# Optimization experiments

Hardware: AMD Instinct MI355X
Metric: run time of the kernel (lower is better)

## Reference

```python
import jax, jax.numpy as jnp
import numpy as np

N = 100000   # nodes
E = 3200000  # edges (avg degree 32)
BN_EPS = 1e-5


def setup_inputs() -> dict:
    key = jax.random.key(0)
    ks = jax.random.split(key, 24)
    w = lambda k, shape: jax.random.normal(k, shape, jnp.float32) * 0.05
    inp = {
        "x": jax.random.normal(ks[0], (N, 1), jnp.float32),
        "edge_index": jax.random.randint(ks[1], (2, E), 0, N, dtype=jnp.int32),
        # GINConv1 mlp1: Linear(1,256) -> BN(256) -> ReLU -> Linear(256,128)
        "w1a": w(ks[2], (1, 256)), "b1a": w(ks[3], (256,)),
        "g1": jnp.ones((256,), jnp.float32), "be1": w(ks[4], (256,)),
        "m1": w(ks[5], (256,)), "v1": jax.random.uniform(ks[6], (256,), jnp.float32, 0.5, 1.5),
        "w1b": w(ks[7], (256, 128)), "b1b": w(ks[8], (128,)),
        # GINConv2 mlp2: Linear(128,64) -> BN(64) -> ReLU -> Linear(64,64)
        "w2a": w(ks[9], (128, 64)), "b2a": w(ks[10], (64,)),
        "g2": jnp.ones((64,), jnp.float32), "be2": w(ks[11], (64,)),
        "m2": w(ks[12], (64,)), "v2": jax.random.uniform(ks[13], (64,), jnp.float32, 0.5, 1.5),
        "w2b": w(ks[14], (64, 64)), "b2b": w(ks[15], (64,)),
        # head: Linear(64,16) -> ReLU -> Linear(16,6) -> log_softmax
        "wl1": w(ks[16], (64, 16)), "bl1": w(ks[17], (16,)),
        "wl2": w(ks[18], (16, 6)), "bl2": w(ks[19], (6,)),
    }
    return inp


def _bn_eval(h, g, b, m, v):
    # BatchNorm1d in eval mode: running stats
    return (h - m) * jax.lax.rsqrt(v + BN_EPS) * g + b


def reference(x, edge_index, w1a, b1a, g1, be1, m1, v1, w1b, b1b,
              w2a, b2a, g2, be2, m2, v2, w2b, b2b, wl1, bl1, wl2, bl2):
    src, dst = edge_index[0], edge_index[1]
    n = x.shape[0]

    def gin(h, mlp):
        # GINConv (eps=0): mlp(h + sum_{j in N(i)} h_j)
        agg = jax.ops.segment_sum(h[src], dst, num_segments=n)
        return mlp(h + agg)

    mlp1 = lambda h: jnp.maximum(_bn_eval(h @ w1a + b1a, g1, be1, m1, v1), 0.0) @ w1b + b1b
    mlp2 = lambda h: jnp.maximum(_bn_eval(h @ w2a + b2a, g2, be2, m2, v2), 0.0) @ w2b + b2b

    x = gin(x, mlp1)   # [N,128]; dropout is identity in eval mode
    x = gin(x, mlp2)   # [N,64]
    x = jnp.maximum(x @ wl1 + bl1, 0.0)  # [N,16]
    x = x @ wl2 + bl2                    # [N,6]
    return jax.nn.log_softmax(x, axis=1)
```

## Files before the change

### kernel.cpp

```cpp
#include <hip/hip_runtime.h>
#include <stdint.h>

#define BN_EPS 1e-5f
#define BW    256
#define BSH   8
#define SLACK 10240
#define TILE  4096

static __device__ __forceinline__ uint32_t bf16bits(float f){
  uint32_t u = __float_as_uint(f);
  return (u + 0x7fffu + ((u>>16)&1u)) >> 16;
}
static __device__ __forceinline__ float bf16tof(uint32_t us){
  return __uint_as_float(us<<16);
}
static __device__ __forceinline__ void acc8(float* acc, uint4 v){
  acc[0]+=bf16tof(v.x&0xFFFFu); acc[1]+=bf16tof(v.x>>16);
  acc[2]+=bf16tof(v.y&0xFFFFu); acc[3]+=bf16tof(v.y>>16);
  acc[4]+=bf16tof(v.z&0xFFFFu); acc[5]+=bf16tof(v.z>>16);
  acc[6]+=bf16tof(v.w&0xFFFFu); acc[7]+=bf16tof(v.w>>16);
}

__global__ __launch_bounds__(256) void prep_small(const float* __restrict__ w1a, const float* __restrict__ b1a,
                           const float* __restrict__ g1,  const float* __restrict__ be1,
                           const float* __restrict__ m1,  const float* __restrict__ v1,
                           const float* __restrict__ b1b, const float* __restrict__ w2a,
                           const float* __restrict__ b2a, const float* __restrict__ g2,
                           const float* __restrict__ be2, const float* __restrict__ m2,
                           const float* __restrict__ v2,
                           float* __restrict__ a1, float* __restrict__ b1v,
                           float* __restrict__ c12, float* __restrict__ A2, float* __restrict__ B2,
                           float* __restrict__ sorted_p, int* __restrict__ perm){
  __shared__ float bpl[256];
  int c = threadIdx.x;
  float s1 = g1[c] * rsqrtf(v1[c] + BN_EPS);
  float av = w1a[c] * s1;
  float bv = (b1a[c] - m1[c]) * s1 + be1[c];
  a1[c]  = av;
  b1v[c] = bv;
  if (c < 64){
    float acc = 0.f;
    for (int d = 0; d < 128; ++d) acc = fmaf(b1b[d], w2a[d*64 + c], acc);
    c12[c] = acc;
    float s2 = g2[c] * rsqrtf(v2[c] + BN_EPS);
    A2[c] = s2;
    B2[c] = (b2a[c] - m2[c]) * s2 + be2[c];
  }
  float bp;
  if (av == 0.f) bp = 1e30f;
  else bp = fminf(fmaxf(-bv/av, -1e30f), 1e30f);
  bpl[c] = bp;
  __syncthreads();
  int rank = 0;
  for (int j = 0; j < 256; ++j){
    float bj = bpl[j];
    rank += (bj < bp) || (bj == bp && j < c);
  }
  sorted_p[rank] = bp;
  perm[rank] = c;
}

__global__ void prep_w12(const float* __restrict__ w1b, const float* __restrict__ w2a,
                         float* __restrict__ W12){
  int idx = blockIdx.x*256 + threadIdx.x;
  int c = idx >> 6, k = idx & 63;
  float acc = 0.f;
  for (int d = 0; d < 128; ++d) acc = fmaf(w1b[c*128 + d], w2a[d*64 + k], acc);
  W12[idx] = acc;
}

__global__ __launch_bounds__(256) void build_ab_par(const float* __restrict__ a1, const float* __restrict__ b1v,
                                                    const float* __restrict__ W12, const float* __restrict__ c12,
                                                    const int* __restrict__ perm, float* __restrict__ AB){
  __shared__ float sm[256];
  int col = blockIdx.x;
  int k = col & 63;
  bool isA = col < 64;
  int tm = threadIdx.x;
  float a0 = a1[tm], b0 = b1v[tm];
  float w0 = W12[tm*64 + k];
  bool act0 = (a0 < 0.f) || (a0 == 0.f && b0 > 0.f);
  float coeff0 = isA ? a0 : b0;
  sm[tm] = act0 ? coeff0*w0 : 0.f;
  __syncthreads();
  for (int off2 = 128; off2 > 0; off2 >>= 1){
    if (tm < off2) sm[tm] += sm[tm + off2];
    __syncthreads();
  }
  float base = sm[0] + (isA ? 0.f : c12[k]);
  __syncthreads();
  int g = perm[tm];
  float ag = a1[g], bg = b1v[g];
  float wg = W12[g*64 + k];
  float cg = isA ? ag : bg;
  float delta = (ag > 0.f) ? cg*wg : ((ag < 0.f) ? -cg*wg : 0.f);
  sm[tm] = delta;
  __syncthreads();
  for (int off = 1; off < 256; off <<= 1){
    float v = (tm >= off) ? sm[tm-off] : 0.f;
    __syncthreads();
    sm[tm] += v;
    __syncthreads();
  }
  AB[(tm+1)*128 + col] = base + sm[tm];
  if (tm == 0) AB[col] = base;
}

__global__ void init_gpos(int* __restrict__ gpos, int nb){
  int i = blockIdx.x*256 + threadIdx.x;
  if (i < nb) gpos[i] = i * SLACK;
}

__global__ __launch_bounds__(512) void bin_edges(const int* __restrict__ ei, int* __restrict__ gpos,
                                                 uint32_t* __restrict__ binned, int E, int nb){
  __shared__ int hist[512];
  __shared__ int sc[512];
  __shared__ int cur[512];
  __shared__ int gbase[512];
  __shared__ uint32_t staged[TILE];
  __shared__ uint16_t bof[TILE];
  int t = threadIdx.x;
  int base = blockIdx.x * TILE;
  hist[t] = 0;
  __syncthreads();
  #pragma unroll
  for (int k = 0; k < TILE/512; ++k){
    int e = base + t + k*512;
    if (e < E) atomicAdd(&hist[ei[E + e] >> BSH], 1);
  }
  __syncthreads();
  int mycnt = hist[t];
  sc[t] = mycnt;
  __syncthreads();
  for (int off = 1; off < 512; off <<= 1){
    int v = (t >= off) ? sc[t-off] : 0;
    __syncthreads();
    sc[t] += v;
    __syncthreads();
  }
  int excl = sc[t] - mycnt;
  hist[t] = excl;
  cur[t]  = excl;
  if (t < nb && mycnt > 0) gbase[t] = atomicAdd(&gpos[t], mycnt);
  __syncthreads();
  #pragma unroll
  for (int k = 0; k < TILE/512; ++k){
    int e = base + t + k*512;
    if (e < E){
      int d = ei[E + e];
      int s = ei[e];
      int b = d >> BSH;
      int slot = atomicAdd(&cur[b], 1);
      staged[slot] = ((uint32_t)(d & (BW-1)) << 17) | (uint32_t)s;
      bof[slot] = (uint16_t)b;
    }
  }
  __syncthreads();
  int tileCount = min(TILE, E - base);
  for (int i = t; i < tileCount; i += 512){
    int b = bof[i];
    binned[gbase[b] + (i - hist[b])] = staged[i];
  }
}

__global__ __launch_bounds__(512) void scan_buckets(const int* __restrict__ gpos, int* __restrict__ bucket_base,
                                                    int* __restrict__ rowstart, int nb, int n, int E){
  __shared__ int sm[512];
  int t = threadIdx.x;
  int c = (t < nb) ? (gpos[t] - t*SLACK) : 0;
  sm[t] = c; __syncthreads();
  for (int off = 1; off < 512; off <<= 1){
    int v = (t >= off) ? sm[t-off] : 0;
    __syncthreads();
    sm[t] += v;
    __syncthreads();
  }
  if (t < nb) bucket_base[t] = sm[t] - c;
  if (t == 0) rowstart[n] = E;
}

__global__ __launch_bounds__(512) void sort_bucket(const uint32_t* __restrict__ binned, const int* __restrict__ gpos,
                                                   const int* __restrict__ bucket_base, int* __restrict__ rowstart,
                                                   int* __restrict__ col, int n){
  __shared__ int hist[BW];
  __shared__ int sc[BW];
  __shared__ int cur[BW];
  int b = blockIdx.x, t = threadIdx.x;
  int cnt = gpos[b] - b*SLACK;
  const uint32_t* src = binned + (size_t)b*SLACK;
  if (t < BW) hist[t] = 0;
  __syncthreads();
  for (int i = t; i < cnt; i += 512) atomicAdd(&hist[src[i] >> 17], 1);
  __syncthreads();
  if (t < BW) sc[t] = hist[t];
  __syncthreads();
  for (int off = 1; off < BW; off <<= 1){
    int v = (t < BW && t >= off) ? sc[t-off] : 0;
    __syncthreads();
    if (t < BW) sc[t] += v;
    __syncthreads();
  }
  int base = bucket_base[b];
  if (t < BW){
    int e = sc[t] - hist[t];
    cur[t] = base + e;
    int node = (b << BSH) + t;
    if (node < n) rowstart[node] = base + e;
  }
  __syncthreads();
  for (int i = t; i < cnt; i += 512){
    uint32_t e = src[i];
    int p = atomicAdd(&cur[e >> 17], 1);
    col[p] = (int)(e & 0x1FFFFu);
  }
}

__global__ __launch_bounds__(256) void gin1_pwl(const float* __restrict__ x,
    const int* __restrict__ rowstart, const int* __restrict__ col,
    const float* __restrict__ sorted_p, const float* __restrict__ AB,
    unsigned short* __restrict__ t, int n){
  __shared__ float sp[256];
  sp[threadIdx.x] = sorted_p[threadIdx.x];
  __syncthreads();
  int tid = blockIdx.x*256 + threadIdx.x;
  int node = tid >> 2, sub = tid & 3;
  if (node >= n) return;
  int beg = rowstart[node], end = rowstart[node+1];
  float s = 0.f;
  for (int j = beg + sub; j < end; j += 4) s += x[col[j]];
  s += __shfl_xor(s, 1);
  s += __shfl_xor(s, 2);
  s += x[node];
  int lo = 0, hi = 256;
  while (lo < hi){
    int mid = (lo + hi) >> 1;
    if (sp[mid] <= s) lo = mid + 1; else hi = mid;
  }
  const float* ab = AB + lo*128 + sub*16;
  const float4* Ap = reinterpret_cast<const float4*>(ab);
  const float4* Bp = reinterpret_cast<const float4*>(ab + 64);
  uint4 o0, o1;
  {
    float4 A0 = Ap[0], A1 = Ap[1], B0 = Bp[0], B1 = Bp[1];
    o0.x = bf16bits(fmaf(A0.x,s,B0.x)) | (bf16bits(fmaf(A0.y,s,B0.y))<<16);
    o0.y = bf16bits(fmaf(A0.z,s,B0.z)) | (bf16bits(fmaf(A0.w,s,B0.w))<<16);
    o0.z = bf16bits(fmaf(A1.x,s,B1.x)) | (bf16bits(fmaf(A1.y,s,B1.y))<<16);
    o0.w = bf16bits(fmaf(A1.z,s,B1.z)) | (bf16bits(fmaf(A1.w,s,B1.w))<<16);
  }
  {
    float4 A2v = Ap[2], A3 = Ap[3], B2v = Bp[2], B3 = Bp[3];
    o1.x = bf16bits(fmaf(A2v.x,s,B2v.x)) | (bf16bits(fmaf(A2v.y,s,B2v.y))<<16);
    o1.y = bf16bits(fmaf(A2v.z,s,B2v.z)) | (bf16bits(fmaf(A2v.w,s,B2v.w))<<16);
    o1.z = bf16bits(fmaf(A3.x,s,B3.x)) | (bf16bits(fmaf(A3.y,s,B3.y))<<16);
    o1.w = bf16bits(fmaf(A3.z,s,B3.z)) | (bf16bits(fmaf(A3.w,s,B3.w))<<16);
  }
  uint4* dst = reinterpret_cast<uint4*>(t + (size_t)node*64 + sub*16);
  dst[0] = o0;
  dst[1] = o1;
}

__global__ __launch_bounds__(256) void agg8(const int* __restrict__ rowstart, const int* __restrict__ col,
                                            const unsigned short* __restrict__ t,
                                            const float* __restrict__ A2, const float* __restrict__ B2,
                                            unsigned short* __restrict__ r2, int n){
  int tid = blockIdx.x*256 + threadIdx.x;
  int lane = threadIdx.x & 63;
  int node = ((tid >> 6) << 3) + (lane >> 3);
  int slot = lane & 7;
  bool valid = node < n;
  int beg = valid ? rowstart[node] : 0;
  int end = valid ? rowstart[node+1] : 0;
  float acc[8];
  {
    const uint4* trow = reinterpret_cast<const uint4*>(t + ((size_t)(valid ? node : 0))*64 + slot*8);
    uint4 v = *trow;
    acc[0]=bf16tof(v.x&0xFFFFu); acc[1]=bf16tof(v.x>>16);
    acc[2]=bf16tof(v.y&0xFFFFu); acc[3]=bf16tof(v.y>>16);
    acc[4]=bf16tof(v.z&0xFFFFu); acc[5]=bf16tof(v.z>>16);
    acc[6]=bf16tof(v.w&0xFFFFu); acc[7]=bf16tof(v.w>>16);
    if (!valid){
      #pragma unroll
      for (int q = 0; q < 8; ++q) acc[q] = 0.f;
    }
  }
  for (int j = beg; __any(j < end); j += 2){
    bool a0 = j < end, a1 = j + 1 < end;
    int s0 = a0 ? col[j] : 0;
    int s1 = a1 ? col[j+1] : 0;
    uint4 w0, w1;
    if (a0) w0 = *reinterpret_cast<const uint4*>(t + (size_t)s0*64 + slot*8);
    if (a1) w1 = *reinterpret_cast<const uint4*>(t + (size_t)s1*64 + slot*8);
    if (a0) acc8(acc, w0);
    if (a1) acc8(acc, w1);
  }
  if (valid){
    const float4* Ap = reinterpret_cast<const float4*>(A2 + slot*8);
    const float4* Bp = reinterpret_cast<const float4*>(B2 + slot*8);
    float4 A0 = Ap[0], A1 = Ap[1], B0 = Bp[0], B1 = Bp[1];
    float Av[8] = {A0.x,A0.y,A0.z,A0.w,A1.x,A1.y,A1.z,A1.w};
    float Bv[8] = {B0.x,B0.y,B0.z,B0.w,B1.x,B1.y,B1.z,B1.w};
    float r[8];
    #pragma unroll
    for (int q = 0; q < 8; ++q) r[q] = fmaxf(fmaf(acc[q], Av[q], Bv[q]), 0.f);
    uint4 o;
    o.x = bf16bits(r[0]) | (bf16bits(r[1])<<16);
    o.y = bf16bits(r[2]) | (bf16bits(r[3])<<16);
    o.z = bf16bits(r[4]) | (bf16bits(r[5])<<16);
    o.w = bf16bits(r[6]) | (bf16bits(r[7])<<16);
    *reinterpret_cast<uint4*>(r2 + (size_t)node*64 + slot*8) = o;
  }
}

__global__ __launch_bounds__(256) void head_kernel(const unsigned short* __restrict__ r2,
    const float* __restrict__ w2b, const float* __restrict__ b2b,
    const float* __restrict__ wl1, const float* __restrict__ bl1,
    const float* __restrict__ wl2, const float* __restrict__ bl2,
    float* __restrict__ out, int n){
  int i = blockIdx.x*256 + threadIdx.x;
  if (i >= n) return;
  float hacc[64];
  #pragma unroll
  for (int k = 0; k < 64; ++k) hacc[k] = b2b[k];
  const uint4* rr = reinterpret_cast<const uint4*>(r2 + (size_t)i*64);
  for (int q = 0; q < 8; ++q){
    uint4 rv = rr[q];
    uint32_t wv[4] = {rv.x, rv.y, rv.z, rv.w};
    #pragma unroll
    for (int e2 = 0; e2 < 4; ++e2){
      float rlo = bf16tof(wv[e2] & 0xFFFFu);
      float rhi = bf16tof(wv[e2] >> 16);
      const float* wr0 = w2b + (q*8 + e2*2)*64;
      #pragma unroll
      for (int k = 0; k < 64; ++k) hacc[k] = fmaf(rlo, wr0[k], hacc[k]);
      const float* wr1 = wr0 + 64;
      #pragma unroll
      for (int k = 0; k < 64; ++k) hacc[k] = fmaf(rhi, wr1[k], hacc[k]);
    }
  }
  float z[16];
  #pragma unroll
  for (int jj = 0; jj < 16; ++jj) z[jj] = bl1[jj];
  #pragma unroll
  for (int k = 0; k < 64; ++k){
    float hk = hacc[k];
    const float* wr = wl1 + k*16;
    #pragma unroll
    for (int jj = 0; jj < 16; ++jj) z[jj] = fmaf(hk, wr[jj], z[jj]);
  }
  float lg[6];
  #pragma unroll
  for (int l = 0; l < 6; ++l) lg[l] = bl2[l];
  #pragma unroll
  for (int jj = 0; jj < 16; ++jj){
    float zj = fmaxf(z[jj], 0.f);
    const float* wr = wl2 + jj*6;
    #pragma unroll
    for (int l = 0; l < 6; ++l) lg[l] = fmaf(zj, wr[l], lg[l]);
  }
  float mx = lg[0];
  #pragma unroll
  for (int l = 1; l < 6; ++l) mx = fmaxf(mx, lg[l]);
  float sum = 0.f;
  #pragma unroll
  for (int l = 0; l < 6; ++l) sum += expf(lg[l] - mx);
  float lse = mx + logf(sum);
  float* op = out + (size_t)i*6;
  #pragma unroll
  for (int l = 0; l < 6; ++l) op[l] = lg[l] - lse;
}

extern "C" void kernel_launch(void* const* d_in, const int* in_sizes, int n_in,
                              void* d_out, int out_size, void* d_ws, size_t ws_size,
                              hipStream_t stream){
  const float* x   = (const float*)d_in[0];
  const int*   ei  = (const int*)d_in[1];
  const float* w1a = (const float*)d_in[2];
  const float* b1a = (const float*)d_in[3];
  const float* g1  = (const float*)d_in[4];
  const float* be1 = (const float*)d_in[5];
  const float* m1  = (const float*)d_in[6];
  const float* v1  = (const float*)d_in[7];
  const float* w1b = (const float*)d_in[8];
  const float* b1b = (const float*)d_in[9];
  const float* w2a = (const float*)d_in[10];
  const float* b2a = (const float*)d_in[11];
  const float* g2  = (const float*)d_in[12];
  const float* be2 = (const float*)d_in[13];
  const float* m2  = (const float*)d_in[14];
  const float* v2  = (const float*)d_in[15];
  const float* w2b = (const float*)d_in[16];
  const float* b2b = (const float*)d_in[17];
  const float* wl1 = (const float*)d_in[18];
  const float* bl1 = (const float*)d_in[19];
  const float* wl2 = (const float*)d_in[20];
  const float* bl2 = (const float*)d_in[21];
  float* out = (float*)d_out;
  int n = in_sizes[0];
  int E = in_sizes[1] / 2;
  int nb = (n + BW - 1) >> BSH;

  char* ws = (char*)d_ws;
  size_t off = 0;
  auto carve = [&](size_t bytes)->char*{ char* p = ws + off; off += (bytes + 255) & ~(size_t)255; return p; };
  float* a1   = (float*)carve(256*4);
  float* b1v  = (float*)carve(256*4);
  float* c12  = (float*)carve(64*4);
  float* A2   = (float*)carve(64*4);
  float* B2   = (float*)carve(64*4);
  float* W12  = (float*)carve(16384*4);
  float* sorted_p = (float*)carve(256*4);
  int*   perm = (int*)carve(256*4);
  float* AB   = (float*)carve(257*128*4);
  int* gpos   = (int*)carve((size_t)nb*4);
  int* bucket_base = (int*)carve((size_t)nb*4);
  int* rowstart = (int*)carve((size_t)(n+1)*4);
  int* col    = (int*)carve((size_t)E*4);
  uint32_t* binned = (uint32_t*)carve((size_t)nb*SLACK*4);
  unsigned short* t  = (unsigned short*)binned;
  unsigned short* r2 = (unsigned short*)carve((size_t)n*64*2);

  int nblk = (n + 255) / 256;
  prep_small<<<1, 256, 0, stream>>>(w1a,b1a,g1,be1,m1,v1,b1b,w2a,b2a,g2,be2,m2,v2,
                                    a1,b1v,c12,A2,B2,sorted_p,perm);
  prep_w12<<<64, 256, 0, stream>>>(w1b, w2a, W12);
  build_ab_par<<<128, 256, 0, stream>>>(a1, b1v, W12, c12, perm, AB);
  init_gpos<<<(nb + 255)/256, 256, 0, stream>>>(gpos, nb);
  bin_edges<<<(E + TILE - 1)/TILE, 512, 0, stream>>>(ei, gpos, binned, E, nb);
  scan_buckets<<<1, 512, 0, stream>>>(gpos, bucket_base, rowstart, nb, n, E);
  sort_bucket<<<nb, 512, 0, stream>>>(binned, gpos, bucket_base, rowstart, col, n);
  gin1_pwl<<<((size_t)n*4 + 255)/256, 256, 0, stream>>>(x, rowstart, col, sorted_p, AB, t, n);
  agg8<<<(n + 31)/32, 256, 0, stream>>>(rowstart, col, t, A2, B2, r2, n);
  head_kernel<<<nblk, 256, 0, stream>>>(r2, w2b, b2b, wl1, bl1, wl2, bl2, out, n);
}
```

Baseline: 309.4 us.

## Store per-node scalar and segment index, recompute layer-1 features during aggregation, fuse head

The first GIN layer now stores only each node's aggregated scalar and its piecewise-linear segment index (8 bytes per node) instead of a 128-byte bf16 feature row. The second aggregation rebuilds each neighbor's 64-wide feature from a small AB table, which cuts gather traffic. The w2b matmul and classifier head are fused into the same kernel using shuffles across 8 lanes, removing the r2 intermediate and the separate head launch. In exchange, each edge needs extra AB table reads and FMAs, the head adds shuffle work, and the intermediate now stays fp32 instead of being rounded to bf16.

```diff
diff --git a/kernel.cpp b/kernel.cpp
--- a/kernel.cpp
+++ b/kernel.cpp
@@ -13,12 +13,6 @@
 }
 static __device__ __forceinline__ float bf16tof(uint32_t us){
   return __uint_as_float(us<<16);
-}
-static __device__ __forceinline__ void acc8(float* acc, uint4 v){
-  acc[0]+=bf16tof(v.x&0xFFFFu); acc[1]+=bf16tof(v.x>>16);
-  acc[2]+=bf16tof(v.y&0xFFFFu); acc[3]+=bf16tof(v.y>>16);
-  acc[4]+=bf16tof(v.z&0xFFFFu); acc[5]+=bf16tof(v.z>>16);
-  acc[6]+=bf16tof(v.w&0xFFFFu); acc[7]+=bf16tof(v.w>>16);
 }
 
 __global__ __launch_bounds__(256) void prep_small(const float* __restrict__ w1a, const float* __restrict__ b1a,
@@ -69,6 +63,12 @@
   W12[idx] = acc;
 }
 
+__global__ void prep_w2bT(const float* __restrict__ w2b, float* __restrict__ w2bT){
+  int idx = blockIdx.x*256 + threadIdx.x;
+  int c = idx >> 6, k = idx & 63;
+  w2bT[k*64 + c] = w2b[c*64 + k];
+}
+
 __global__ __launch_bounds__(256) void build_ab_par(const float* __restrict__ a1, const float* __restrict__ b1v,
                                                     const float* __restrict__ W12, const float* __restrict__ c12,
                                                     const int* __restrict__ perm, float* __restrict__ AB){
@@ -215,10 +215,9 @@
   }
 }
 
-__global__ __launch_bounds__(256) void gin1_pwl(const float* __restrict__ x,
+__global__ __launch_bounds__(256) void gin1_ms(const float* __restrict__ x,
     const int* __restrict__ rowstart, const int* __restrict__ col,
-    const float* __restrict__ sorted_p, const float* __restrict__ AB,
-    unsigned short* __restrict__ t, int n){
+    const float* __restrict__ sorted_p, uint2* __restrict__ ms, int n){
   __shared__ float sp[256];
   sp[threadIdx.x] = sorted_p[threadIdx.x];
   __syncthreads();
@@ -231,129 +230,129 @@
   s += __shfl_xor(s, 1);
   s += __shfl_xor(s, 2);
   s += x[node];
-  int lo = 0, hi = 256;
-  while (lo < hi){
-    int mid = (lo + hi) >> 1;
-    if (sp[mid] <= s) lo = mid + 1; else hi = mid;
-  }
-  const float* ab = AB + lo*128 + sub*16;
-  const float4* Ap = reinterpret_cast<const float4*>(ab);
-  const float4* Bp = reinterpret_cast<const float4*>(ab + 64);
-  uint4 o0, o1;
-  {
-    float4 A0 = Ap[0], A1 = Ap[1], B0 = Bp[0], B1 = Bp[1];
-    o0.x = bf16bits(fmaf(A0.x,s,B0.x)) | (bf16bits(fmaf(A0.y,s,B0.y))<<16);
-    o0.y = bf16bits(fmaf(A0.z,s,B0.z)) | (bf16bits(fmaf(A0.w,s,B0.w))<<16);
-    o0.z = bf16bits(fmaf(A1.x,s,B1.x)) | (bf16bits(fmaf(A1.y,s,B1.y))<<16);
-    o0.w = bf16bits(fmaf(A1.z,s,B1.z)) | (bf16bits(fmaf(A1.w,s,B1.w))<<16);
-  }
-  {
-    float4 A2v = Ap[2], A3 = Ap[3], B2v = Bp[2], B3 = Bp[3];
-    o1.x = bf16bits(fmaf(A2v.x,s,B2v.x)) | (bf16bits(fmaf(A2v.y,s,B2v.y))<<16);
-    o1.y = bf16bits(fmaf(A2v.z,s,B2v.z)) | (bf16bits(fmaf(A2v.w,s,B2v.w))<<16);
-    o1.z = bf16bits(fmaf(A3.x,s,B3.x)) | (bf16bits(fmaf(A3.y,s,B3.y))<<16);
-    o1.w = bf16bits(fmaf(A3.z,s,B3.z)) | (bf16bits(fmaf(A3.w,s,B3.w))<<16);
-  }
-  uint4* dst = reinterpret_cast<uint4*>(t + (size_t)node*64 + sub*16);
-  dst[0] = o0;
-  dst[1] = o1;
-}
-
-__global__ __launch_bounds__(256) void agg8(const int* __restrict__ rowstart, const int* __restrict__ col,
-                                            const unsigned short* __restrict__ t,
-                                            const float* __restrict__ A2, const float* __restrict__ B2,
-                                            unsigned short* __restrict__ r2, int n){
+  if (sub == 0){
+    int lo = 0, hi = 256;
+    while (lo < hi){
+      int mid = (lo + hi) >> 1;
+      if (sp[mid] <= s) lo = mid + 1; else hi = mid;
+    }
+    uint2 v; v.x = __float_as_uint(s); v.y = (uint32_t)lo;
+    ms[node] = v;
+  }
+}
+
+static __device__ __forceinline__ void accAB(float* u, const float* __restrict__ AB,
+                                             uint2 mv, int slot){
+  float s = __uint_as_float(mv.x);
+  const float4* ap = reinterpret_cast<const float4*>(AB + (size_t)mv.y*128 + slot*8);
+  const float4* bp = reinterpret_cast<const float4*>(AB + (size_t)mv.y*128 + 64 + slot*8);
+  float4 a0 = ap[0], a1 = ap[1], b0 = bp[0], b1 = bp[1];
+  u[0] += fmaf(a0.x, s, b0.x);
+  u[1] += fmaf(a0.y, s, b0.y);
+  u[2] += fmaf(a0.z, s, b0.z);
+  u[3] += fmaf(a0.w, s, b0.w);
+  u[4] += fmaf(a1.x, s, b1.x);
+  u[5] += fmaf(a1.y, s, b1.y);
+  u[6] += fmaf(a1.z, s, b1.z);
+  u[7] += fmaf(a1.w, s, b1.w);
+}
+
+__global__ __launch_bounds__(256) void agg_ms(const int* __restrict__ rowstart, const int* __restrict__ col,
+    const uint2* __restrict__ ms, const float* __restrict__ AB,
+    const float* __restrict__ A2, const float* __restrict__ B2,
+    const float* __restrict__ w2bT, const float* __restrict__ b2b,
+    const float* __restrict__ wl1, const float* __restrict__ bl1,
+    const float* __restrict__ wl2, const float* __restrict__ bl2,
+    float* __restrict__ out, int n){
   int tid = blockIdx.x*256 + threadIdx.x;
   int lane = threadIdx.x & 63;
   int node = ((tid >> 6) << 3) + (lane >> 3);
   int slot = lane & 7;
   bool valid = node < n;
-  int beg = valid ? rowstart[node] : 0;
-  int end = valid ? rowstart[node+1] : 0;
-  float acc[8];
-  {
-    const uint4* trow = reinterpret_cast<const uint4*>(t + ((size_t)(valid ? node : 0))*64 + slot*8);
-    uint4 v = *trow;
-    acc[0]=bf16tof(v.x&0xFFFFu); acc[1]=bf16tof(v.x>>16);
-    acc[2]=bf16tof(v.y&0xFFFFu); acc[3]=bf16tof(v.y>>16);
-    acc[4]=bf16tof(v.z&0xFFFFu); acc[5]=bf16tof(v.z>>16);
-    acc[6]=bf16tof(v.w&0xFFFFu); acc[7]=bf16tof(v.w>>16);
-    if (!valid){
-      #pragma unroll
-      for (int q = 0; q < 8; ++q) acc[q] = 0.f;
-    }
-  }
+  int nd = valid ? node : 0;
+  int beg = rowstart[nd];
+  int end = valid ? rowstart[nd+1] : beg;
+  float u[8];
+  #pragma unroll
+  for (int q = 0; q < 8; ++q) u[q] = 0.f;
+  accAB(u, AB, ms[nd], slot);
   for (int j = beg; __any(j < end); j += 2){
     bool a0 = j < end, a1 = j + 1 < end;
-    int s0 = a0 ? col[j] : 0;
-    int s1 = a1 ? col[j+1] : 0;
-    uint4 w0, w1;
-    if (a0) w0 = *reinterpret_cast<const uint4*>(t + (size_t)s0*64 + slot*8);
-    if (a1) w1 = *reinterpret_cast<const uint4*>(t + (size_t)s1*64 + slot*8);
-    if (a0) acc8(acc, w0);
-    if (a1) acc8(acc, w1);
-  }
-  if (valid){
+    int c0 = a0 ? col[j] : 0;
+    int c1 = a1 ? col[j+1] : 0;
+    uint2 m0, m1;
+    if (a0) m0 = ms[c0];
+    if (a1) m1 = ms[c1];
+    if (a0) accAB(u, AB, m0, slot);
+    if (a1) accAB(u, AB, m1, slot);
+  }
+  {
     const float4* Ap = reinterpret_cast<const float4*>(A2 + slot*8);
     const float4* Bp = reinterpret_cast<const float4*>(B2 + slot*8);
     float4 A0 = Ap[0], A1 = Ap[1], B0 = Bp[0], B1 = Bp[1];
-    float Av[8] = {A0.x,A0.y,A0.z,A0.w,A1.x,A1.y,A1.z,A1.w};
-    float Bv[8] = {B0.x,B0.y,B0.z,B0.w,B1.x,B1.y,B1.z,B1.w};
-    float r[8];
+    u[0] = fmaxf(fmaf(u[0], A0.x, B0.x), 0.f);
+    u[1] = fmaxf(fmaf(u[1], A0.y, B0.y), 0.f);
+    u[2] = fmaxf(fmaf(u[2], A0.z, B0.z), 0.f);
+    u[3] = fmaxf(fmaf(u[3], A0.w, B0.w), 0.f);
+    u[4] = fmaxf(fmaf(u[4], A1.x, B1.x), 0.f);
+    u[5] = fmaxf(fmaf(u[5], A1.y, B1.y), 0.f);
+    u[6] = fmaxf(fmaf(u[6], A1.z, B1.z), 0.f);
+    u[7] = fmaxf(fmaf(u[7], A1.w, B1.w), 0.f);
+  }
+  float h8[8];
+  #pragma unroll
+  for (int q = 0; q < 8; ++q) h8[q] = 0.f;
+  #pragma unroll
+  for (int rot = 0; rot < 8; ++rot){
+    int src = slot ^ rot;
+    float rv0 = __shfl(u[0], src, 8);
+    float rv1 = __shfl(u[1], src, 8);
+    float rv2 = __shfl(u[2], src, 8);
+    float rv3 = __shfl(u[3], src, 8);
+    float rv4 = __shfl(u[4], src, 8);
+    float rv5 = __shfl(u[5], src, 8);
+    float rv6 = __shfl(u[6], src, 8);
+    float rv7 = __shfl(u[7], src, 8);
+    int cbase = src*8;
     #pragma unroll
-    for (int q = 0; q < 8; ++q) r[q] = fmaxf(fmaf(acc[q], Av[q], Bv[q]), 0.f);
-    uint4 o;
-    o.x = bf16bits(r[0]) | (bf16bits(r[1])<<16);
-    o.y = bf16bits(r[2]) | (bf16bits(r[3])<<16);
-    o.z = bf16bits(r[4]) | (bf16bits(r[5])<<16);
-    o.w = bf16bits(r[6]) | (bf16bits(r[7])<<16);
-    *reinterpret_cast<uint4*>(r2 + (size_t)node*64 + slot*8) = o;
-  }
-}
-
-__global__ __launch_bounds__(256) void head_kernel(const unsigned short* __restrict__ r2,
-    const float* __restrict__ w2b, const float* __restrict__ b2b,
-    const float* __restrict__ wl1, const float* __restrict__ bl1,
-    const float* __restrict__ wl2, const float* __restrict__ bl2,
-    float* __restrict__ out, int n){
-  int i = blockIdx.x*256 + threadIdx.x;
-  if (i >= n) return;
-  float hacc[64];
-  #pragma unroll
-  for (int k = 0; k < 64; ++k) hacc[k] = b2b[k];
-  const uint4* rr = reinterpret_cast<const uint4*>(r2 + (size_t)i*64);
-  for (int q = 0; q < 8; ++q){
-    uint4 rv = rr[q];
-    uint32_t wv[4] = {rv.x, rv.y, rv.z, rv.w};
+    for (int kk = 0; kk < 8; ++kk){
+      const float4* wp = reinterpret_cast<const float4*>(w2bT + (size_t)(slot*8+kk)*64 + cbase);
+      float4 wa = wp[0], wb = wp[1];
+      h8[kk] += rv0*wa.x + rv1*wa.y + rv2*wa.z + rv3*wa.w
+              + rv4*wb.x + rv5*wb.y + rv6*wb.z + rv7*wb.w;
+    }
+  }
+  {
+    const float4* bb = reinterpret_cast<const float4*>(b2b + slot*8);
+    float4 b0 = bb[0], b1 = bb[1];
+    h8[0]+=b0.x; h8[1]+=b0.y; h8[2]+=b0.z; h8[3]+=b0.w;
+    h8[4]+=b1.x; h8[5]+=b1.y; h8[6]+=b1.z; h8[7]+=b1.w;
+  }
+  float z16[16];
+  #pragma unroll
+  for (int j = 0; j < 16; ++j) z16[j] = 0.f;
+  #pragma unroll
+  for (int kk = 0; kk < 8; ++kk){
+    float hk = h8[kk];
+    const float4* wr = reinterpret_cast<const float4*>(wl1 + (size_t)(slot*8+kk)*16);
+    float4 w0 = wr[0], w1 = wr[1], w2 = wr[2], w3 = wr[3];
+    z16[0]+=hk*w0.x;  z16[1]+=hk*w0.y;  z16[2]+=hk*w0.z;  z16[3]+=hk*w0.w;
+    z16[4]+=hk*w1.x;  z16[5]+=hk*w1.y;  z16[6]+=hk*w1.z;  z16[7]+=hk*w1.w;
+    z16[8]+=hk*w2.x;  z16[9]+=hk*w2.y;  z16[10]+=hk*w2.z; z16[11]+=hk*w2.w;
+    z16[12]+=hk*w3.x; z16[13]+=hk*w3.y; z16[14]+=hk*w3.z; z16[15]+=hk*w3.w;
+  }
+  #pragma unroll
+  for (int mask = 1; mask < 8; mask <<= 1){
     #pragma unroll
-    for (int e2 = 0; e2 < 4; ++e2){
-      float rlo = bf16tof(wv[e2] & 0xFFFFu);
-      float rhi = bf16tof(wv[e2] >> 16);
-      const float* wr0 = w2b + (q*8 + e2*2)*64;
-      #pragma unroll
-      for (int k = 0; k < 64; ++k) hacc[k] = fmaf(rlo, wr0[k], hacc[k]);
-      const float* wr1 = wr0 + 64;
-      #pragma unroll
-      for (int k = 0; k < 64; ++k) hacc[k] = fmaf(rhi, wr1[k], hacc[k]);
-    }
-  }
-  float z[16];
-  #pragma unroll
-  for (int jj = 0; jj < 16; ++jj) z[jj] = bl1[jj];
-  #pragma unroll
-  for (int k = 0; k < 64; ++k){
-    float hk = hacc[k];
-    const float* wr = wl1 + k*16;
-    #pragma unroll
-    for (int jj = 0; jj < 16; ++jj) z[jj] = fmaf(hk, wr[jj], z[jj]);
+    for (int j = 0; j < 16; ++j) z16[j] += __shfl_xor(z16[j], mask);
   }
   float lg[6];
   #pragma unroll
   for (int l = 0; l < 6; ++l) lg[l] = bl2[l];
   #pragma unroll
-  for (int jj = 0; jj < 16; ++jj){
-    float zj = fmaxf(z[jj], 0.f);
-    const float* wr = wl2 + jj*6;
+  for (int j = 0; j < 16; ++j){
+    float zj = fmaxf(z16[j] + bl1[j], 0.f);
+    const float* wr = wl2 + j*6;
     #pragma unroll
     for (int l = 0; l < 6; ++l) lg[l] = fmaf(zj, wr[l], lg[l]);
   }
@@ -364,9 +363,13 @@
   #pragma unroll
   for (int l = 0; l < 6; ++l) sum += expf(lg[l] - mx);
   float lse = mx + logf(sum);
-  float* op = out + (size_t)i*6;
-  #pragma unroll
-  for (int l = 0; l < 6; ++l) op[l] = lg[l] - lse;
+  float vout = lg[0];
+  vout = (slot == 1) ? lg[1] : vout;
+  vout = (slot == 2) ? lg[2] : vout;
+  vout = (slot == 3) ? lg[3] : vout;
+  vout = (slot == 4) ? lg[4] : vout;
+  vout = (slot == 5) ? lg[5] : vout;
+  if (valid && slot < 6) out[(size_t)node*6 + slot] = vout - lse;
 }
 
 extern "C" void kernel_launch(void* const* d_in, const int* in_sizes, int n_in,
@@ -408,6 +411,7 @@
   float* A2   = (float*)carve(64*4);
   float* B2   = (float*)carve(64*4);
   float* W12  = (float*)carve(16384*4);
+  float* w2bT = (float*)carve(4096*4);
   float* sorted_p = (float*)carve(256*4);
   int*   perm = (int*)carve(256*4);
   float* AB   = (float*)carve(257*128*4);
@@ -416,19 +420,18 @@
   int* rowstart = (int*)carve((size_t)(n+1)*4);
   int* col    = (int*)carve((size_t)E*4);
   uint32_t* binned = (uint32_t*)carve((size_t)nb*SLACK*4);
-  unsigned short* t  = (unsigned short*)binned;
-  unsigned short* r2 = (unsigned short*)carve((size_t)n*64*2);
-
-  int nblk = (n + 255) / 256;
+  uint2* ms   = (uint2*)carve((size_t)n*8);
+
   prep_small<<<1, 256, 0, stream>>>(w1a,b1a,g1,be1,m1,v1,b1b,w2a,b2a,g2,be2,m2,v2,
                                     a1,b1v,c12,A2,B2,sorted_p,perm);
   prep_w12<<<64, 256, 0, stream>>>(w1b, w2a, W12);
+  prep_w2bT<<<16, 256, 0, stream>>>(w2b, w2bT);
   build_ab_par<<<128, 256, 0, stream>>>(a1, b1v, W12, c12, perm, AB);
   init_gpos<<<(nb + 255)/256, 256, 0, stream>>>(gpos, nb);
   bin_edges<<<(E + TILE - 1)/TILE, 512, 0, stream>>>(ei, gpos, binned, E, nb);
   scan_buckets<<<1, 512, 0, stream>>>(gpos, bucket_base, rowstart, nb, n, E);
   sort_bucket<<<nb, 512, 0, stream>>>(binned, gpos, bucket_base, rowstart, col, n);
-  gin1_pwl<<<((size_t)n*4 + 255)/256, 256, 0, stream>>>(x, rowstart, col, sorted_p, AB, t, n);
-  agg8<<<(n + 31)/32, 256, 0, stream>>>(rowstart, col, t, A2, B2, r2, n);
-  head_kernel<<<nblk, 256, 0, stream>>>(r2, w2b, b2b, wl1, bl1, wl2, bl2, out, n);
-}
+  gin1_ms<<<((size_t)n*4 + 255)/256, 256, 0, stream>>>(x, rowstart, col, sorted_p, ms, n);
+  agg_ms<<<(n + 31)/32, 256, 0, stream>>>(rowstart, col, ms, AB, A2, B2,
+                                          w2bT, b2b, wl1, bl1, wl2, bl2, out, n);
+}
```

After: 417.2 us. +34.9%, slower.
